# Performance work log

Hardware: AMD Instinct MI355X
Metric: run time of the kernel (lower is better)

The kernel has to match this reference:

```python
import jax, jax.numpy as jnp
import numpy as np

B, S, E, H, D, R = 2, 2048, 1024, 16, 64, 16


def setup_inputs() -> dict:
    key = jax.random.key(0)
    ks = jax.random.split(key, 9)
    s = lambda k, shape, fan: jax.random.normal(k, shape, dtype=jnp.float32) / np.sqrt(fan)
    return {
        "x": jax.random.normal(ks[0], (B, S, E), dtype=jnp.float32),
        "Wq": s(ks[1], (H, E, D), E),
        "bq": jnp.zeros((H, D), jnp.float32),
        "Wk": s(ks[2], (H, E, D), E),
        "bk": jnp.zeros((H, D), jnp.float32),
        "Wvd": s(ks[3], (H, E, R), E),
        "bvd": jnp.zeros((H, R), jnp.float32),
        "Wvu": s(ks[4], (H, R, D), R),
        "bvu": jnp.zeros((H, D), jnp.float32),
    }


def reference(x, Wq, bq, Wk, bk, Wvd, bvd, Wvu, bvu):
    b, s, e = x.shape
    # per-head projections, vectorized over heads h
    q = jnp.einsum('bse,hed->bhsd', x, Wq) + bq[None, :, None, :]
    k = jnp.einsum('bse,hed->bhsd', x, Wk) + bk[None, :, None, :]
    # NOTE: original scales by sqrt(embedding_dimension), not head dim
    scores = jnp.einsum('bhsd,bhtd->bhst', q, k) / jnp.sqrt(jnp.float32(e))
    # original mask: masked_fill where key_idx < query_idx (anti-causal)
    qi = jnp.arange(s)[:, None]
    ki = jnp.arange(s)[None, :]
    scores = jnp.where(ki < qi, -jnp.inf, scores)
    att = jax.nn.softmax(scores, axis=-1)  # dropout p=0 (eval)
    # low-rank value: up(down(x))
    vd = jnp.einsum('bse,her->bhsr', x, Wvd) + bvd[None, :, None, :]
    v = jnp.einsum('bhsr,hrd->bhsd', vd, Wvu) + bvu[None, :, None, :]
    out = jnp.einsum('bhst,bhtd->bhsd', att, v)
    # concat heads along last dim (head order = stack order)
    return out.transpose(0, 2, 1, 3).reshape(b, s, -1)
```

## Files before the change

### kernel.cpp

```cpp
#include <hip/hip_runtime.h>
#include <stdint.h>

#define B_ 2
#define S_ 2048
#define E_ 1024
#define H_ 16
#define D_ 64
#define R_ 16

typedef short s16x8 __attribute__((ext_vector_type(8)));
typedef short s16x4 __attribute__((ext_vector_type(4)));
typedef float f32x4 __attribute__((ext_vector_type(4)));

__device__ __forceinline__ unsigned short f2bf(float f) {
  union { float f; unsigned u; } v; v.f = f;
  return (unsigned short)((v.u + 0x8000u) >> 16);
}

__device__ __forceinline__ void load_lds16(const void* g, void* l) {
  __builtin_amdgcn_global_load_lds(
      (__attribute__((address_space(1))) void*)(g),
      (__attribute__((address_space(3))) void*)(l), 16, 0, 0);
}

__global__ void k_prep(const float* __restrict__ x,
                       const float* __restrict__ Wq, const float* __restrict__ Wk,
                       const float* __restrict__ Wvd, const float* __restrict__ Wvu,
                       const float* __restrict__ bq, const float* __restrict__ bk,
                       const float* __restrict__ bvd, const float* __restrict__ bvu,
                       unsigned short* __restrict__ xb, unsigned short* __restrict__ Wt,
                       float* __restrict__ ball) {
  __shared__ float T[64][65];
  const int blk = blockIdx.x;
  const int t = threadIdx.x;
  if (blk < 4096) {
    int i = (blk * 256 + t) * 4;
    float4 v = *(const float4*)(x + i);
    ushort4 o;
    o.x = f2bf(v.x); o.y = f2bf(v.y); o.z = f2bf(v.z); o.w = f2bf(v.w);
    *(ushort4*)(xb + i) = o;
  } else if (blk < 4608) {
    const int bb = blk - 4096;
    const int which = bb >> 8;
    const int h = (bb >> 4) & 15;
    const int et = bb & 15;
    const float* src = (which ? Wk : Wq) + (h * E_ + et * 64) * D_;
#pragma unroll
    for (int pr = 0; pr < 4; ++pr) {
      const int row = pr * 16 + (t >> 4);
      const int col = (t & 15) * 4;
      float4 v = *(const float4*)(src + row * 64 + col);
      T[row][col] = v.x; T[row][col + 1] = v.y; T[row][col + 2] = v.z; T[row][col + 3] = v.w;
    }
    __syncthreads();
#pragma unroll
    for (int pr = 0; pr < 4; ++pr) {
      const int d = pr * 16 + (t >> 4);
      const int ec = (t & 15) * 4;
      ushort4 o;
      o.x = f2bf(T[ec][d]); o.y = f2bf(T[ec + 1][d]);
      o.z = f2bf(T[ec + 2][d]); o.w = f2bf(T[ec + 3][d]);
      *(ushort4*)(Wt + ((which << 10) + h * 64 + d) * 1024 + et * 64 + ec) = o;
    }
  } else if (blk < 8704) {
    const int idx = (blk - 4608) * 256 + t;
    const int row = idx >> 10;
    const int e = idx & 1023;
    const int h = row >> 6, d = row & 63;
    const float4* wd4 = (const float4*)(Wvd + (h << 14) + e * 16);
    const float* wu = Wvu + h * R_ * D_ + d;
    float acc = 0.f;
#pragma unroll
    for (int r4 = 0; r4 < 4; ++r4) {
      float4 a = wd4[r4];
      acc += a.x * wu[(r4 * 4 + 0) * 64];
      acc += a.y * wu[(r4 * 4 + 1) * 64];
      acc += a.z * wu[(r4 * 4 + 2) * 64];
      acc += a.w * wu[(r4 * 4 + 3) * 64];
    }
    Wt[(2048 + row) * 1024 + e] = f2bf(acc);
  } else {
    int n = (blk - 8704) * 256 + t;
    int which = n >> 10;
    int hd = n & 1023;
    int h = hd >> 6, d = hd & 63;
    float v;
    if (which == 0) v = bq[hd];
    else if (which == 1) v = bk[hd];
    else {
      v = bvu[hd];
#pragma unroll
      for (int r = 0; r < R_; ++r) v += bvd[h * R_ + r] * Wvu[(h * R_ + r) * D_ + d];
    }
    ball[n] = v;
  }
}


__global__ __launch_bounds__(256, 2) void k_gemm_qkv(
    const unsigned short* __restrict__ X, const unsigned short* __restrict__ Wt,
    const float* __restrict__ ball,
    unsigned short* __restrict__ Qb, unsigned short* __restrict__ Kb,
    unsigned short* __restrict__ Vb) {
  __shared__ unsigned short As[128 * 32];
  __shared__ unsigned short Bs[128 * 32];
  const int tid = threadIdx.x;
  const int lane = tid & 63, wave = tid >> 6;
  const int quad = lane >> 4, l16 = lane & 15;
  const int mBase = blockIdx.y * 128, nBase = blockIdx.x * 128;
  const int wm = (wave & 1) * 64, wn = (wave >> 1) * 64;
  const int lrow = lane >> 2, lcol = (lane & 3) * 8;

  f32x4 acc[4][4];
#pragma unroll
  for (int mi = 0; mi < 4; ++mi)
#pragma unroll
    for (int ni = 0; ni < 4; ++ni) acc[mi][ni] = (f32x4){0.f, 0.f, 0.f, 0.f};

  for (int k0 = 0; k0 < E_; k0 += 32) {
#pragma unroll
    for (int i = 0; i < 2; ++i) {
      const int r0 = __builtin_amdgcn_readfirstlane((wave + i * 4) * 16);
      load_lds16(X + (mBase + r0 + lrow) * E_ + k0 + lcol, &As[r0 * 32]);
      load_lds16(Wt + (nBase + r0 + lrow) * E_ + k0 + lcol, &Bs[r0 * 32]);
    }
    __syncthreads();
    s16x8 af[4], bfr[4];
#pragma unroll
    for (int mi = 0; mi < 4; ++mi)
      af[mi] = *(const s16x8*)&As[(wm + mi * 16 + l16) * 32 + quad * 8];
#pragma unroll
    for (int ni = 0; ni < 4; ++ni)
      bfr[ni] = *(const s16x8*)&Bs[(wn + ni * 16 + l16) * 32 + quad * 8];
#pragma unroll
    for (int mi = 0; mi < 4; ++mi)
#pragma unroll
      for (int ni = 0; ni < 4; ++ni)
        acc[mi][ni] = __builtin_amdgcn_mfma_f32_16x16x32_bf16(af[mi], bfr[ni], acc[mi][ni], 0, 0, 0);
    __syncthreads();
  }

  const int which = nBase >> 10;
#pragma unroll
  for (int ni = 0; ni < 4; ++ni) {
    const int n = nBase + wn + ni * 16 + l16;
    const int nh = n & 1023;
    const int h = nh >> 6, d = nh & 63;
    const float bias = ball[n];
#pragma unroll
    for (int mi = 0; mi < 4; ++mi) {
      const int m0 = mBase + wm + mi * 16 + quad * 4;
      const int b = m0 >> 11;
      const int s = m0 & 2047;
      const int bh = b * H_ + h;
      if (which == 2) {
        ushort4 pk;
        pk.x = f2bf(acc[mi][ni][0] + bias);
        pk.y = f2bf(acc[mi][ni][1] + bias);
        pk.z = f2bf(acc[mi][ni][2] + bias);
        pk.w = f2bf(acc[mi][ni][3] + bias);
        *(ushort4*)(Vb + (bh * D_ + d) * S_ + s) = pk;
      } else {
        unsigned short* dst = (which == 0 ? Qb : Kb) + (bh * S_ + s) * D_ + d;
#pragma unroll
        for (int r = 0; r < 4; ++r) dst[r * D_] = f2bf(acc[mi][ni][r] + bias);
      }
    }
  }
}


struct QState {
  s16x8 qf[2];
  f32x4 o[4];
  float l[4];
};

__device__ __forceinline__ void attn_tile(
    QState& st, const unsigned short* Ksb, const unsigned short* Vsb,
    unsigned short* myPs, int quad, int l16, int wave, bool diag) {
  const float K1 = 1.44269504f / 32.f;
  const float K0 = -28.8539008f;
  f32x4 sc[4];
#pragma unroll
  for (int tc = 0; tc < 4; ++tc) {
    f32x4 a = (f32x4){0.f, 0.f, 0.f, 0.f};
#pragma unroll
    for (int dc = 0; dc < 2; ++dc) {
      s16x8 kb = *(const s16x8*)&Ksb[dc * 2048 + (tc * 16 + l16) * 32 + quad * 8];
      a = __builtin_amdgcn_mfma_f32_16x16x32_bf16(st.qf[dc], kb, a, 0, 0, 0);
    }
    sc[tc] = a;
  }
  if (diag) {
#pragma unroll
    for (int tc = 0; tc < 4; ++tc)
#pragma unroll
      for (int r = 0; r < 4; ++r) {
        const int t = tc * 16 + l16;
        const int q = wave * 16 + quad * 4 + r;
        if (t < q) sc[tc][r] = -3.0e38f;
      }
  }
#pragma unroll
  for (int tc = 0; tc < 4; ++tc)
#pragma unroll
    for (int r = 0; r < 4; ++r) {
      float p = exp2f(fmaf(sc[tc][r], K1, K0));
      st.l[r] += p;
      myPs[(tc >> 1) * 576 + (quad * 4 + r) * 36 + (tc & 1) * 16 + l16] = f2bf(p);
    }
#pragma unroll
  for (int dc = 0; dc < 4; ++dc) {
#pragma unroll
    for (int kc = 0; kc < 2; ++kc) {
      s16x4 plo = *(const s16x4*)&myPs[kc * 576 + l16 * 36 + quad * 8];
      s16x4 phi = *(const s16x4*)&myPs[kc * 576 + l16 * 36 + quad * 8 + 4];
      s16x8 pf = __builtin_shufflevector(plo, phi, 0, 1, 2, 3, 4, 5, 6, 7);
      s16x8 vb = *(const s16x8*)&Vsb[kc * 2048 + (dc * 16 + l16) * 32 + quad * 8];
      st.o[dc] = __builtin_amdgcn_mfma_f32_16x16x32_bf16(pf, vb, st.o[dc], 0, 0, 0);
    }
  }
}

__global__ __launch_bounds__(256, 2) void k_attn(
    const unsigned short* __restrict__ Qb, const unsigned short* __restrict__ Kb,
    const unsigned short* __restrict__ Vb, float* __restrict__ out) {
  __shared__ unsigned short Ks[2][2 * 64 * 32];
  __shared__ unsigned short Vs[2][2 * 64 * 32];
  __shared__ unsigned short Ps[4 * 2 * 16 * 36];
  const int tid = threadIdx.x;
  const int lane = tid & 63, wave = tid >> 6;
  const int quad = lane >> 4, l16 = lane & 15;
  const int bh = blockIdx.x & 31;
  const int pt = blockIdx.x >> 5;
  const int qa = pt, qb = 31 - pt;
  const int lrow = lane >> 2, lcol = (lane & 3) * 8;
  const int r0 = __builtin_amdgcn_readfirstlane(wave * 16);

  QState A, Bt;
  {
    const unsigned short* qp = Qb + (bh * S_ + qa * 64 + wave * 16 + l16) * D_ + quad * 8;
    A.qf[0] = *(const s16x8*)qp;
    A.qf[1] = *(const s16x8*)(qp + 32);
    const unsigned short* qp2 = Qb + (bh * S_ + qb * 64 + wave * 16 + l16) * D_ + quad * 8;
    Bt.qf[0] = *(const s16x8*)qp2;
    Bt.qf[1] = *(const s16x8*)(qp2 + 32);
  }
#pragma unroll
  for (int dc = 0; dc < 4; ++dc) {
    A.o[dc] = (f32x4){0.f, 0.f, 0.f, 0.f};
    Bt.o[dc] = (f32x4){0.f, 0.f, 0.f, 0.f};
  }
#pragma unroll
  for (int r = 0; r < 4; ++r) { A.l[r] = 0.f; Bt.l[r] = 0.f; }

  unsigned short* myPs = &Ps[wave * 1152];

#pragma unroll
  for (int hdc = 0; hdc < 2; ++hdc) {
    load_lds16(Kb + (bh * S_ + qa * 64 + r0 + lrow) * D_ + hdc * 32 + lcol,
               &Ks[0][hdc * 2048 + r0 * 32]);
    load_lds16(Vb + (bh * D_ + r0 + lrow) * S_ + qa * 64 + hdc * 32 + lcol,
               &Vs[0][hdc * 2048 + r0 * 32]);
  }

  int buf = 0;
  for (int kt = qa; kt < 32; ++kt) {
    __syncthreads();
    if (kt + 1 < 32) {
      const int k0n = (kt + 1) * 64;
#pragma unroll
      for (int hdc = 0; hdc < 2; ++hdc) {
        load_lds16(Kb + (bh * S_ + k0n + r0 + lrow) * D_ + hdc * 32 + lcol,
                   &Ks[buf ^ 1][hdc * 2048 + r0 * 32]);
        load_lds16(Vb + (bh * D_ + r0 + lrow) * S_ + k0n + hdc * 32 + lcol,
                   &Vs[buf ^ 1][hdc * 2048 + r0 * 32]);
      }
    }
    attn_tile(A, Ks[buf], Vs[buf], myPs, quad, l16, wave, kt == qa);
    if (kt >= qb) attn_tile(Bt, Ks[buf], Vs[buf], myPs, quad, l16, wave, kt == qb);
    buf ^= 1;
  }

#pragma unroll
  for (int off = 1; off < 16; off <<= 1)
#pragma unroll
    for (int r = 0; r < 4; ++r) {
      A.l[r] += __shfl_xor(A.l[r], off);
      Bt.l[r] += __shfl_xor(Bt.l[r], off);
    }
  const int b = bh >> 4, h = bh & 15;
#pragma unroll
  for (int r = 0; r < 4; ++r) {
    const float ra = 1.f / A.l[r], rb = 1.f / Bt.l[r];
    const int sa = qa * 64 + wave * 16 + quad * 4 + r;
    const int sb = qb * 64 + wave * 16 + quad * 4 + r;
#pragma unroll
    for (int dc = 0; dc < 4; ++dc) {
      out[(b * S_ + sa) * (H_ * D_) + h * D_ + dc * 16 + l16] = A.o[dc][r] * ra;
      out[(b * S_ + sb) * (H_ * D_) + h * D_ + dc * 16 + l16] = Bt.o[dc][r] * rb;
    }
  }
}


extern "C" void kernel_launch(void* const* d_in, const int* in_sizes, int n_in,
                              void* d_out, int out_size, void* d_ws, size_t ws_size,
                              hipStream_t stream) {
  const float* x   = (const float*)d_in[0];
  const float* Wq  = (const float*)d_in[1];
  const float* bq  = (const float*)d_in[2];
  const float* Wk  = (const float*)d_in[3];
  const float* bk  = (const float*)d_in[4];
  const float* Wvd = (const float*)d_in[5];
  const float* bvd = (const float*)d_in[6];
  const float* Wvu = (const float*)d_in[7];
  const float* bvu = (const float*)d_in[8];
  float* out = (float*)d_out;

  char* ws = (char*)d_ws;
  unsigned short* xb   = (unsigned short*)(ws);
  unsigned short* Wt   = (unsigned short*)(ws + (8u << 20));
  float*          ball = (float*)(ws + (14u << 20));
  unsigned short* Qb   = (unsigned short*)(ws + (15u << 20));
  unsigned short* Kb   = (unsigned short*)(ws + (23u << 20));
  unsigned short* Vb   = (unsigned short*)(ws + (31u << 20));

  k_prep<<<8716, 256, 0, stream>>>(x, Wq, Wk, Wvd, Wvu, bq, bk, bvd, bvu, xb, Wt, ball);
  k_gemm_qkv<<<dim3(3072 / 128, 4096 / 128), 256, 0, stream>>>(xb, Wt, ball, Qb, Kb, Vb);
  k_attn<<<512, 256, 0, stream>>>(Qb, Kb, Vb, out);
}
```

Measured before the change: 173.3 us.

## Restructure attention: split key tiles across waves, fold scale into Wq, direct global loads

Folds the softmax scale and log2e factor into Wq and bq during prep, and feeds the exp2 offset in as the initial MFMA accumulator, so the per-score FMA disappears. The attention kernel drops the paired light/heavy query tile scheme and the LDS double-buffered K/V staging. It now launches one block per 64-query tile, with each wave taking 32 queries and half of each key tile, loading K/V fragments straight from global memory. Partial outputs and row sums from the two key halves are merged through LDS at the end. It also uses truncation instead of rounding for the P bf16 conversion and raises occupancy to 3 blocks per SM, at the risk of load imbalance across query tiles and uncached global reads.

```diff
diff --git a/kernel.cpp b/kernel.cpp
--- a/kernel.cpp
+++ b/kernel.cpp
@@ -9,8 +9,10 @@
 #define R_ 16
 
 typedef short s16x8 __attribute__((ext_vector_type(8)));
-typedef short s16x4 __attribute__((ext_vector_type(4)));
 typedef float f32x4 __attribute__((ext_vector_type(4)));
+
+#define K1_ 0.045084220027780106f
+#define K0_ -28.853900817779268f
 
 __device__ __forceinline__ unsigned short f2bf(float f) {
   union { float f; unsigned u; } v; v.f = f;
@@ -44,6 +46,7 @@
     const int which = bb >> 8;
     const int h = (bb >> 4) & 15;
     const int et = bb & 15;
+    const float scl = which ? 1.f : K1_;
     const float* src = (which ? Wk : Wq) + (h * E_ + et * 64) * D_;
 #pragma unroll
     for (int pr = 0; pr < 4; ++pr) {
@@ -58,8 +61,8 @@
       const int d = pr * 16 + (t >> 4);
       const int ec = (t & 15) * 4;
       ushort4 o;
-      o.x = f2bf(T[ec][d]); o.y = f2bf(T[ec + 1][d]);
-      o.z = f2bf(T[ec + 2][d]); o.w = f2bf(T[ec + 3][d]);
+      o.x = f2bf(T[ec][d] * scl); o.y = f2bf(T[ec + 1][d] * scl);
+      o.z = f2bf(T[ec + 2][d] * scl); o.w = f2bf(T[ec + 3][d] * scl);
       *(ushort4*)(Wt + ((which << 10) + h * 64 + d) * 1024 + et * 64 + ec) = o;
     }
   } else if (blk < 8704) {
@@ -85,7 +88,7 @@
     int hd = n & 1023;
     int h = hd >> 6, d = hd & 63;
     float v;
-    if (which == 0) v = bq[hd];
+    if (which == 0) v = bq[hd] * K1_;
     else if (which == 1) v = bk[hd];
     else {
       v = bvu[hd];
@@ -170,136 +173,142 @@
 }
 
 
-struct QState {
-  s16x8 qf[2];
-  f32x4 o[4];
-  float l[4];
-};
-
-__device__ __forceinline__ void attn_tile(
-    QState& st, const unsigned short* Ksb, const unsigned short* Vsb,
-    unsigned short* myPs, int quad, int l16, int wave, bool diag) {
-  const float K1 = 1.44269504f / 32.f;
-  const float K0 = -28.8539008f;
-  f32x4 sc[4];
-#pragma unroll
-  for (int tc = 0; tc < 4; ++tc) {
-    f32x4 a = (f32x4){0.f, 0.f, 0.f, 0.f};
-#pragma unroll
-    for (int dc = 0; dc < 2; ++dc) {
-      s16x8 kb = *(const s16x8*)&Ksb[dc * 2048 + (tc * 16 + l16) * 32 + quad * 8];
-      a = __builtin_amdgcn_mfma_f32_16x16x32_bf16(st.qf[dc], kb, a, 0, 0, 0);
-    }
-    sc[tc] = a;
-  }
-  if (diag) {
-#pragma unroll
-    for (int tc = 0; tc < 4; ++tc)
-#pragma unroll
-      for (int r = 0; r < 4; ++r) {
-        const int t = tc * 16 + l16;
-        const int q = wave * 16 + quad * 4 + r;
-        if (t < q) sc[tc][r] = -3.0e38f;
-      }
-  }
-#pragma unroll
-  for (int tc = 0; tc < 4; ++tc)
-#pragma unroll
-    for (int r = 0; r < 4; ++r) {
-      float p = exp2f(fmaf(sc[tc][r], K1, K0));
-      st.l[r] += p;
-      myPs[(tc >> 1) * 576 + (quad * 4 + r) * 36 + (tc & 1) * 16 + l16] = f2bf(p);
-    }
-#pragma unroll
-  for (int dc = 0; dc < 4; ++dc) {
-#pragma unroll
-    for (int kc = 0; kc < 2; ++kc) {
-      s16x4 plo = *(const s16x4*)&myPs[kc * 576 + l16 * 36 + quad * 8];
-      s16x4 phi = *(const s16x4*)&myPs[kc * 576 + l16 * 36 + quad * 8 + 4];
-      s16x8 pf = __builtin_shufflevector(plo, phi, 0, 1, 2, 3, 4, 5, 6, 7);
-      s16x8 vb = *(const s16x8*)&Vsb[kc * 2048 + (dc * 16 + l16) * 32 + quad * 8];
-      st.o[dc] = __builtin_amdgcn_mfma_f32_16x16x32_bf16(pf, vb, st.o[dc], 0, 0, 0);
-    }
-  }
-}
-
-__global__ __launch_bounds__(256, 2) void k_attn(
+__global__ __launch_bounds__(256, 3) void k_attn(
     const unsigned short* __restrict__ Qb, const unsigned short* __restrict__ Kb,
     const unsigned short* __restrict__ Vb, float* __restrict__ out) {
-  __shared__ unsigned short Ks[2][2 * 64 * 32];
-  __shared__ unsigned short Vs[2][2 * 64 * 32];
-  __shared__ unsigned short Ps[4 * 2 * 16 * 36];
+  __shared__ unsigned short Ps[4][2][16][40];
+  __shared__ float obuf[2][64][36];
+  __shared__ float lbuf[64];
   const int tid = threadIdx.x;
   const int lane = tid & 63, wave = tid >> 6;
   const int quad = lane >> 4, l16 = lane & 15;
+  const int tHalf = wave >> 1, qHalf = wave & 1;
+  const int qt = blockIdx.x >> 5;
   const int bh = blockIdx.x & 31;
-  const int pt = blockIdx.x >> 5;
-  const int qa = pt, qb = 31 - pt;
-  const int lrow = lane >> 2, lcol = (lane & 3) * 8;
-  const int r0 = __builtin_amdgcn_readfirstlane(wave * 16);
-
-  QState A, Bt;
-  {
-    const unsigned short* qp = Qb + (bh * S_ + qa * 64 + wave * 16 + l16) * D_ + quad * 8;
-    A.qf[0] = *(const s16x8*)qp;
-    A.qf[1] = *(const s16x8*)(qp + 32);
-    const unsigned short* qp2 = Qb + (bh * S_ + qb * 64 + wave * 16 + l16) * D_ + quad * 8;
-    Bt.qf[0] = *(const s16x8*)qp2;
-    Bt.qf[1] = *(const s16x8*)(qp2 + 32);
-  }
-#pragma unroll
-  for (int dc = 0; dc < 4; ++dc) {
-    A.o[dc] = (f32x4){0.f, 0.f, 0.f, 0.f};
-    Bt.o[dc] = (f32x4){0.f, 0.f, 0.f, 0.f};
-  }
-#pragma unroll
-  for (int r = 0; r < 4; ++r) { A.l[r] = 0.f; Bt.l[r] = 0.f; }
-
-  unsigned short* myPs = &Ps[wave * 1152];
-
-#pragma unroll
-  for (int hdc = 0; hdc < 2; ++hdc) {
-    load_lds16(Kb + (bh * S_ + qa * 64 + r0 + lrow) * D_ + hdc * 32 + lcol,
-               &Ks[0][hdc * 2048 + r0 * 32]);
-    load_lds16(Vb + (bh * D_ + r0 + lrow) * S_ + qa * 64 + hdc * 32 + lcol,
-               &Vs[0][hdc * 2048 + r0 * 32]);
-  }
-
-  int buf = 0;
-  for (int kt = qa; kt < 32; ++kt) {
-    __syncthreads();
-    if (kt + 1 < 32) {
-      const int k0n = (kt + 1) * 64;
-#pragma unroll
-      for (int hdc = 0; hdc < 2; ++hdc) {
-        load_lds16(Kb + (bh * S_ + k0n + r0 + lrow) * D_ + hdc * 32 + lcol,
-                   &Ks[buf ^ 1][hdc * 2048 + r0 * 32]);
-        load_lds16(Vb + (bh * D_ + r0 + lrow) * S_ + k0n + hdc * 32 + lcol,
-                   &Vs[buf ^ 1][hdc * 2048 + r0 * 32]);
+  const f32x4 kvec = {K0_, K0_, K0_, K0_};
+
+  s16x8 qf[2][2];
+#pragma unroll
+  for (int m = 0; m < 2; ++m)
+#pragma unroll
+    for (int dc = 0; dc < 2; ++dc)
+      qf[m][dc] = *(const s16x8*)(Qb +
+          (bh * S_ + qt * 64 + qHalf * 32 + m * 16 + l16) * D_ + dc * 32 + quad * 8);
+
+  f32x4 o[2][4];
+#pragma unroll
+  for (int m = 0; m < 2; ++m)
+#pragma unroll
+    for (int dc = 0; dc < 4; ++dc) o[m][dc] = (f32x4){0.f, 0.f, 0.f, 0.f};
+  float l_acc[2][2][4];
+#pragma unroll
+  for (int m = 0; m < 2; ++m)
+#pragma unroll
+    for (int nt = 0; nt < 2; ++nt)
+#pragma unroll
+      for (int r = 0; r < 4; ++r) l_acc[m][nt][r] = 0.f;
+
+  for (int kt = qt; kt < S_ / 64; ++kt) {
+    const int tBase = kt * 64 + tHalf * 32;
+    s16x8 kb[2][2];
+#pragma unroll
+    for (int nt = 0; nt < 2; ++nt)
+#pragma unroll
+      for (int dc = 0; dc < 2; ++dc)
+        kb[nt][dc] = *(const s16x8*)(Kb +
+            (bh * S_ + tBase + nt * 16 + l16) * D_ + dc * 32 + quad * 8);
+    s16x8 vb[4];
+#pragma unroll
+    for (int dc = 0; dc < 4; ++dc)
+      vb[dc] = *(const s16x8*)(Vb +
+          (bh * D_ + dc * 16 + l16) * S_ + tBase + quad * 8);
+
+    f32x4 sc[2][2];
+#pragma unroll
+    for (int m = 0; m < 2; ++m)
+#pragma unroll
+      for (int nt = 0; nt < 2; ++nt) {
+        f32x4 a = __builtin_amdgcn_mfma_f32_16x16x32_bf16(qf[m][0], kb[nt][0], kvec, 0, 0, 0);
+        sc[m][nt] = __builtin_amdgcn_mfma_f32_16x16x32_bf16(qf[m][1], kb[nt][1], a, 0, 0, 0);
       }
-    }
-    attn_tile(A, Ks[buf], Vs[buf], myPs, quad, l16, wave, kt == qa);
-    if (kt >= qb) attn_tile(Bt, Ks[buf], Vs[buf], myPs, quad, l16, wave, kt == qb);
-    buf ^= 1;
-  }
-
+
+    if (kt == qt) {
+#pragma unroll
+      for (int m = 0; m < 2; ++m)
+#pragma unroll
+        for (int nt = 0; nt < 2; ++nt)
+#pragma unroll
+          for (int r = 0; r < 4; ++r) {
+            const int t = tHalf * 32 + nt * 16 + l16;
+            const int q = qHalf * 32 + m * 16 + quad * 4 + r;
+            if (t < q) sc[m][nt][r] = -200.f;
+          }
+    }
+
+#pragma unroll
+    for (int m = 0; m < 2; ++m)
+#pragma unroll
+      for (int nt = 0; nt < 2; ++nt)
+#pragma unroll
+        for (int r = 0; r < 4; ++r) {
+          float p = exp2f(sc[m][nt][r]);
+          l_acc[m][nt][r] += p;
+          Ps[wave][m][quad * 4 + r][nt * 16 + l16] =
+              (unsigned short)(__float_as_uint(p) >> 16);
+        }
+
+#pragma unroll
+    for (int m = 0; m < 2; ++m) {
+      s16x8 pf = *(const s16x8*)&Ps[wave][m][l16][quad * 8];
+#pragma unroll
+      for (int dc = 0; dc < 4; ++dc)
+        o[m][dc] = __builtin_amdgcn_mfma_f32_16x16x32_bf16(pf, vb[dc], o[m][dc], 0, 0, 0);
+    }
+  }
+
+  float lr[2][4];
+#pragma unroll
+  for (int m = 0; m < 2; ++m)
+#pragma unroll
+    for (int r = 0; r < 4; ++r) lr[m][r] = l_acc[m][0][r] + l_acc[m][1][r];
 #pragma unroll
   for (int off = 1; off < 16; off <<= 1)
 #pragma unroll
-    for (int r = 0; r < 4; ++r) {
-      A.l[r] += __shfl_xor(A.l[r], off);
-      Bt.l[r] += __shfl_xor(Bt.l[r], off);
-    }
-  const int b = bh >> 4, h = bh & 15;
-#pragma unroll
-  for (int r = 0; r < 4; ++r) {
-    const float ra = 1.f / A.l[r], rb = 1.f / Bt.l[r];
-    const int sa = qa * 64 + wave * 16 + quad * 4 + r;
-    const int sb = qb * 64 + wave * 16 + quad * 4 + r;
-#pragma unroll
-    for (int dc = 0; dc < 4; ++dc) {
-      out[(b * S_ + sa) * (H_ * D_) + h * D_ + dc * 16 + l16] = A.o[dc][r] * ra;
-      out[(b * S_ + sb) * (H_ * D_) + h * D_ + dc * 16 + l16] = Bt.o[dc][r] * rb;
+    for (int m = 0; m < 2; ++m)
+#pragma unroll
+      for (int r = 0; r < 4; ++r) lr[m][r] += __shfl_xor(lr[m][r], off);
+
+  if (tHalf == 1) {
+#pragma unroll
+    for (int m = 0; m < 2; ++m)
+#pragma unroll
+      for (int dc = 0; dc < 4; ++dc)
+        *(f32x4*)&obuf[qHalf][dc * 16 + l16][m * 16 + quad * 4] = o[m][dc];
+    if (l16 == 0) {
+#pragma unroll
+      for (int m = 0; m < 2; ++m)
+        *(float4*)&lbuf[qHalf * 32 + m * 16 + quad * 4] =
+            make_float4(lr[m][0], lr[m][1], lr[m][2], lr[m][3]);
+    }
+  }
+  __syncthreads();
+  if (tHalf == 0) {
+    const int b = bh >> 4, h = bh & 15;
+#pragma unroll
+    for (int m = 0; m < 2; ++m) {
+      float rinv[4];
+#pragma unroll
+      for (int r = 0; r < 4; ++r)
+        rinv[r] = 1.f / (lr[m][r] + lbuf[qHalf * 32 + m * 16 + quad * 4 + r]);
+#pragma unroll
+      for (int dc = 0; dc < 4; ++dc) {
+        f32x4 oo = o[m][dc] + *(const f32x4*)&obuf[qHalf][dc * 16 + l16][m * 16 + quad * 4];
+#pragma unroll
+        for (int r = 0; r < 4; ++r) {
+          const int s = qt * 64 + qHalf * 32 + m * 16 + quad * 4 + r;
+          out[(b * S_ + s) * (H_ * D_) + h * D_ + dc * 16 + l16] = oo[r] * rinv[r];
+        }
+      }
     }
   }
 }
@@ -329,5 +338,5 @@
 
   k_prep<<<8716, 256, 0, stream>>>(x, Wq, Wk, Wvd, Wvu, bq, bk, bvd, bvu, xb, Wt, ball);
   k_gemm_qkv<<<dim3(3072 / 128, 4096 / 128), 256, 0, stream>>>(xb, Wt, ball, Qb, Kb, Vb);
-  k_attn<<<512, 256, 0, stream>>>(Qb, Kb, Vb, out);
-}
+  k_attn<<<1024, 256, 0, stream>>>(Qb, Kb, Vb, out);
+}
```

Result: slower. 195.4 us (+12.8%).
